# Kernel optimization log

Hardware: AMD Instinct MI355X
Metric: run time of the kernel (lower is better)

Reference implementation:

```python
import jax, jax.numpy as jnp
import numpy as np

L, HID, NH, DH, OUT = 20, 512, 8, 64, 1000
NPAT, PS = 14, 16
IN_DIM = 3 * PS * PS          # 768
SEQ = NPAT * NPAT + 1         # 197
BATCH = 64
EPS = 1e-5


def _pos_embeddings(seq_len, d):
    # sin(i/10000^(j/d)) for even j, cos(i/10000^((j-1)/d)) for odd j
    i = jnp.arange(seq_len, dtype=jnp.float32)[:, None]
    j = jnp.arange(d)
    je = (j - (j % 2)).astype(jnp.float32)
    ang = i / jnp.power(10000.0, je / d)
    return jnp.where(j % 2 == 0, jnp.sin(ang), jnp.cos(ang))


def _layernorm(x, g, b):
    m = jnp.mean(x, axis=-1, keepdims=True)
    v = jnp.mean(jnp.square(x - m), axis=-1, keepdims=True)
    return (x - m) * jax.lax.rsqrt(v + EPS) * g + b


def setup_inputs() -> dict:
    key = jax.random.key(0)
    ks = jax.random.split(key, 12)
    r = lambda k, sh: jax.random.normal(k, sh, dtype=jnp.float32) * 0.02
    return {
        "x": jax.random.normal(ks[0], (BATCH, 3, 224, 224), dtype=jnp.float32),
        "embed_W": r(ks[1], (IN_DIM, HID)),
        "embed_b": jnp.zeros((HID,), jnp.float32),
        "cls": r(ks[2], (HID,)),
        "ln1_g": jnp.ones((L, HID), jnp.float32),
        "ln1_b": jnp.zeros((L, HID), jnp.float32),
        "qW": r(ks[3], (L, NH, DH, DH)),
        "qb": jnp.zeros((L, NH, DH), jnp.float32),
        "kW": r(ks[4], (L, NH, DH, DH)),
        "kb": jnp.zeros((L, NH, DH), jnp.float32),
        "vW": r(ks[5], (L, NH, DH, DH)),
        "vb": jnp.zeros((L, NH, DH), jnp.float32),
        "ln2_g": jnp.ones((L, HID), jnp.float32),
        "ln2_b": jnp.zeros((L, HID), jnp.float32),
        "mlp1_W": r(ks[6], (L, HID, 4 * HID)),
        "mlp1_b": jnp.zeros((L, 4 * HID), jnp.float32),
        "mlp2_W": r(ks[7], (L, 4 * HID, HID)),
        "mlp2_b": jnp.zeros((L, HID), jnp.float32),
        "head_W": r(ks[8], (HID, OUT)),
        "head_b": jnp.zeros((OUT,), jnp.float32),
    }


def reference(x, embed_W, embed_b, cls, ln1_g, ln1_b, qW, qb, kW, kb, vW, vb,
              ln2_g, ln2_b, mlp1_W, mlp1_b, mlp2_W, mlp2_b, head_W, head_b):
    n = x.shape[0]
    # patchify: [n,3,224,224] -> [n,196,768], flatten order (c, ph, pw)
    p = x.reshape(n, 3, NPAT, PS, NPAT, PS)
    p = p.transpose(0, 2, 4, 1, 3, 5).reshape(n, NPAT * NPAT, IN_DIM)
    tokens = p @ embed_W + embed_b                      # [n,196,HID]
    cls_tok = jnp.broadcast_to(cls, (n, 1, HID))
    h = jnp.concatenate([cls_tok, tokens], axis=1)      # [n,197,HID]
    h = h + _pos_embeddings(SEQ, HID)

    scale = 1.0 / jnp.sqrt(jnp.float32(DH))

    def step(h, params):
        (g1, b1, qw, qb_, kw, kb_, vw, vb_, g2, b2, w1, b1m, w2, b2m) = params
        y = _layernorm(h, g1, b1)                       # [n,S,HID]
        yh = y.reshape(n, SEQ, NH, DH)
        # torch Linear: out = seq @ W.T + b; qw stored as [NH, out, in]
        q = jnp.einsum('nshd,hed->nshe', yh, qw) + qb_
        k = jnp.einsum('nshd,hed->nshe', yh, kw) + kb_
        v = jnp.einsum('nshd,hed->nshe', yh, vw) + vb_
        att = jax.nn.softmax(jnp.einsum('nqhd,nkhd->nhqk', q, k) * scale, axis=-1)
        o = jnp.einsum('nhqk,nkhd->nqhd', att, v).reshape(n, SEQ, HID)
        h = h + o
        z = _layernorm(h, g2, b2)
        z = jax.nn.gelu(z @ w1 + b1m, approximate=False) @ w2 + b2m
        return h + z, None

    params = (ln1_g, ln1_b, qW, qb, kW, kb, vW, vb,
              ln2_g, ln2_b, mlp1_W, mlp1_b, mlp2_W, mlp2_b)
    h, _ = jax.lax.scan(step, h, params)
    logits = h[:, 0] @ head_W + head_b
    return jax.nn.softmax(logits, axis=-1)
```

## Files before the change

### kernel.cpp

```cpp
#include <hip/hip_runtime.h>
#include <hip/hip_bf16.h>
#include <math.h>

#define LAY 20
#define HID 512
#define NH 8
#define DH 64
#define OUTC 1000
#define SEQ 197
#define SPAD 224
#define BATCH 64
#define TT (BATCH*SEQ)
#define M2 12800
#define NPTOK (BATCH*196)
#define IN_DIM 768

typedef __attribute__((ext_vector_type(8))) short bf16x8;
typedef __attribute__((ext_vector_type(4))) float f32x4;

__device__ __forceinline__ ushort f2bf(float f){
  __hip_bfloat16 h = __float2bfloat16(f);
  return *(ushort*)&h;
}
__device__ __forceinline__ float bf2f(ushort u){
  __hip_bfloat16 h = *(__hip_bfloat16*)&u;
  return __bfloat162float(h);
}

__device__ __forceinline__ float posemb(int i, int j){
  float je = (float)(j & ~1);
  float ang = (float)i * powf(10000.0f, -je * (1.0f/(float)HID));
  return (j & 1) ? cosf(ang) : sinf(ang);
}

__device__ __forceinline__ float gelu_exact(float x){
  return 0.5f * x * (1.0f + erff(x * 0.70710678118654752f));
}

__device__ __forceinline__ void gld_lds16(const ushort* g, ushort* l){
  __builtin_amdgcn_global_load_lds((const __attribute__((address_space(1))) void*)g,
                                   (__attribute__((address_space(3))) void*)l, 16, 0, 0);
}

__global__ __launch_bounds__(512)
void pos_kernel(float* __restrict__ pos){
  int i = blockIdx.x, j = threadIdx.x;
  pos[(size_t)i*HID + j] = posemb(i, j);
}

__global__ __launch_bounds__(256)
void convt_kernel(const float* __restrict__ src, ushort* __restrict__ dst,
                  int R, int C){
  __shared__ float tile[32][33];
  const float* s = src + (size_t)blockIdx.z * R * C;
  ushort* d      = dst + (size_t)blockIdx.z * R * C;
  int r0 = blockIdx.y * 32, c0 = blockIdx.x * 32;
  int tc = threadIdx.x & 31, tr = threadIdx.x >> 5;
  #pragma unroll
  for (int i = 0; i < 4; ++i)
    tile[tr + i*8][tc] = s[(size_t)(r0 + tr + i*8)*C + c0 + tc];
  __syncthreads();
  #pragma unroll
  for (int i = 0; i < 4; ++i)
    d[(size_t)(c0 + tr + i*8)*R + r0 + tc] = f2bf(tile[tc][tr + i*8]);
}

__global__ __launch_bounds__(256)
void cvt_kernel(const float* __restrict__ src, ushort* __restrict__ dst, int count){
  int idx = blockIdx.x * 256 + threadIdx.x;
  if (idx < count) dst[idx] = f2bf(src[idx]);
}

__global__ __launch_bounds__(256)
void patchify_kernel(const float* __restrict__ x, ushort* __restrict__ p){
  int idx = blockIdx.x * 256 + threadIdx.x;
  int r   = idx / 768, cdx = idx - r * 768;
  int n   = r / 196,  pp  = r - n * 196;
  int pr  = pp / 14,  pc  = pp - pr * 14;
  int c   = cdx >> 8, rem = cdx & 255;
  int ph  = rem >> 4, pw  = rem & 15;
  p[idx] = f2bf(x[ (((size_t)(n*3 + c)*224) + pr*16 + ph)*224 + pc*16 + pw ]);
}

__global__ __launch_bounds__(512)
void cls_kernel(const float* __restrict__ cls, const float* __restrict__ pos,
                float* __restrict__ h){
  int n = blockIdx.x, e = threadIdx.x;
  h[(size_t)n*SEQ*HID + e] = cls[e] + pos[e];
}

template<int BN, int EPI>
__global__ __launch_bounds__(256, 4)
void gemm_pipe(const ushort* __restrict__ A, const ushort* __restrict__ Bt,
               const float* __restrict__ bias, void* __restrict__ Cv,
               int K, int N, int Mreal, int NBX, const float* __restrict__ pos){
  constexpr int BM = 128;
  constexpr int MF = 4, NF = BN/32;
  constexpr int BQ = BN/64;
  constexpr int TBS = 8192 + BN*64;
  constexpr int ES = NF*16 + 12;
  __shared__ char lds[2*TBS];

  int t = threadIdx.x, lane = t & 63, wave = t >> 6;
  int wr = wave >> 1, wn = wave & 1;
  int l16 = lane & 15, g = lane >> 4;

  int NB = gridDim.x;
  int q8 = NB >> 3, r8 = NB & 7;
  int xcd = blockIdx.x & 7, i8 = blockIdx.x >> 3;
  int swz = (xcd < r8 ? xcd*(q8+1) : r8*(q8+1) + (xcd-r8)*q8) + i8;
  int rb = (swz / NBX) * BM, cb = (swz % NBX) * BN;

  const int srow = t >> 2;
  const int kel  = ((t & 3) ^ ((srow >> 1) & 3)) * 8;
  const ushort* pA[2]; const ushort* pB[BQ];
  #pragma unroll
  for (int q = 0; q < 2; ++q)
    pA[q] = A + (size_t)(rb + q*64 + srow)*K + kel;
  #pragma unroll
  for (int q = 0; q < BQ; ++q)
    pB[q] = Bt + (size_t)(cb + q*64 + srow)*K + kel;
  const int sdst = t*16;

  const int sx = (l16 >> 1) & 3;
  int aoff[MF], boff[NF];
  #pragma unroll
  for (int mf = 0; mf < MF; ++mf)
    aoff[mf] = (wr*64 + mf*16 + l16)*64 + ((g ^ sx) << 4);
  #pragma unroll
  for (int nf = 0; nf < NF; ++nf)
    boff[nf] = 8192 + (wn*(NF*16) + nf*16 + l16)*64 + ((g ^ sx) << 4);

  f32x4 acc[MF][NF];
  #pragma unroll
  for (int mf = 0; mf < MF; ++mf)
    #pragma unroll
    for (int nf = 0; nf < NF; ++nf)
      acc[mf][nf] = (f32x4){0.f,0.f,0.f,0.f};

  #pragma unroll
  for (int q = 0; q < 2; ++q)
    gld_lds16(pA[q], (ushort*)(lds + q*4096 + sdst));
  #pragma unroll
  for (int q = 0; q < BQ; ++q)
    gld_lds16(pB[q], (ushort*)(lds + 8192 + q*4096 + sdst));

  int NT = K / 32;
  for (int tt = 0; tt < NT; ++tt){
    const char* cur = lds + (tt & 1)*TBS;
    char* nxt = lds + ((tt & 1) ^ 1)*TBS;
    bool pf = (tt + 1 < NT);
    if (pf){
      const size_t kb = (size_t)(tt + 1) * 32;
      #pragma unroll
      for (int q = 0; q < 2; ++q)
        gld_lds16(pA[q] + kb, (ushort*)(nxt + q*4096 + sdst));
      #pragma unroll
      for (int q = 0; q < BQ; ++q)
        gld_lds16(pB[q] + kb, (ushort*)(nxt + 8192 + q*4096 + sdst));
      if constexpr (BQ == 2)
        asm volatile("s_waitcnt vmcnt(4)" ::: "memory");
      else
        asm volatile("s_waitcnt vmcnt(3)" ::: "memory");
    } else {
      asm volatile("s_waitcnt vmcnt(0)" ::: "memory");
    }
    __builtin_amdgcn_s_barrier();

    bf16x8 af[MF], bfr[NF];
    #pragma unroll
    for (int nf = 0; nf < NF; ++nf)
      bfr[nf] = *(const bf16x8*)(cur + boff[nf]);
    #pragma unroll
    for (int mf = 0; mf < MF; ++mf)
      af[mf] = *(const bf16x8*)(cur + aoff[mf]);

    __builtin_amdgcn_s_setprio(1);
    #pragma unroll
    for (int mf = 0; mf < MF; ++mf)
      #pragma unroll
      for (int nf = 0; nf < NF; ++nf)
        acc[mf][nf] = __builtin_amdgcn_mfma_f32_16x16x32_bf16(af[mf], bfr[nf], acc[mf][nf], 0, 0, 0);
    __builtin_amdgcn_s_setprio(0);
    __builtin_amdgcn_s_barrier();
  }

  float bvv[NF];
  #pragma unroll
  for (int nf = 0; nf < NF; ++nf)
    bvv[nf] = bias[cb + wn*(NF*16) + nf*16 + l16];
  float* eps = (float*)(lds + wave*(16*ES*4));

  #pragma unroll
  for (int mf = 0; mf < MF; ++mf){
    #pragma unroll
    for (int nf = 0; nf < NF; ++nf)
      #pragma unroll
      for (int j = 0; j < 4; ++j){
        float val = acc[mf][nf][j] + bvv[nf];
        if (EPI == 1) val = gelu_exact(val);
        eps[(g*4+j)*ES + nf*16 + l16] = val;
      }
    #pragma unroll
    for (int i = 0; i < NF; ++i){
      int id = i*64 + lane;
      int r = id / (4*NF), c4 = id % (4*NF);
      float4 vv = *(float4*)&eps[r*ES + c4*4];
      int grow = rb + wr*64 + mf*16 + r;
      int gcol = cb + wn*(NF*16) + c4*4;
      if (EPI == 1){
        ushort4 u;
        u.x = f2bf(vv.x); u.y = f2bf(vv.y); u.z = f2bf(vv.z); u.w = f2bf(vv.w);
        *(ushort4*)&((ushort*)Cv)[(size_t)grow*N + gcol] = u;
      } else if (EPI == 2){
        if (grow < Mreal){
          float* cp = &((float*)Cv)[(size_t)grow*N + gcol];
          float4 o = *(float4*)cp;
          o.x += vv.x; o.y += vv.y; o.z += vv.z; o.w += vv.w;
          *(float4*)cp = o;
        }
      } else {
        if (grow < Mreal){
          int bn = grow / 196, sp = grow - bn*196;
          float4 pv = *(const float4*)&pos[(size_t)(1+sp)*HID + gcol];
          vv.x += pv.x; vv.y += pv.y; vv.z += pv.z; vv.w += pv.w;
          *(float4*)&((float*)Cv)[((size_t)bn*SEQ + 1 + sp)*HID + gcol] = vv;
        }
      }
    }
  }
}

__global__ __launch_bounds__(128)
void ln_kernel(const float* __restrict__ x, const float* __restrict__ g,
               const float* __restrict__ b, ushort* __restrict__ y){
  int tok = blockIdx.x, t = threadIdx.x;
  int wave = t >> 6;
  __shared__ float red[2];
  float4 v = *(const float4*)&x[(size_t)tok*HID + t*4];
  float s = (v.x + v.y) + (v.z + v.w);
  #pragma unroll
  for (int off = 32; off; off >>= 1) s += __shfl_xor(s, off);
  if ((t & 63) == 0) red[wave] = s;
  __syncthreads();
  float mean = (red[0] + red[1]) * (1.0f/512.0f);
  __syncthreads();
  float dx = v.x - mean, dy = v.y - mean, dz = v.z - mean, dw = v.w - mean;
  s = (dx*dx + dy*dy) + (dz*dz + dw*dw);
  #pragma unroll
  for (int off = 32; off; off >>= 1) s += __shfl_xor(s, off);
  if ((t & 63) == 0) red[wave] = s;
  __syncthreads();
  float var = (red[0] + red[1]) * (1.0f/512.0f);
  float rs  = rsqrtf(var + 1e-5f);
  float4 gv = *(const float4*)&g[t*4];
  float4 bv = *(const float4*)&b[t*4];
  ushort4 o;
  o.x = f2bf(dx*rs*gv.x + bv.x);
  o.y = f2bf(dy*rs*gv.y + bv.y);
  o.z = f2bf(dz*rs*gv.z + bv.z);
  o.w = f2bf(dw*rs*gv.w + bv.w);
  *(ushort4*)&y[(size_t)tok*HID + t*4] = o;
}

__global__ __launch_bounds__(256)
void qkv_mfma(const ushort* __restrict__ y,
              const ushort* __restrict__ wqb, const ushort* __restrict__ wkb,
              const ushort* __restrict__ wvb,
              const float* __restrict__ bq, const float* __restrict__ bk,
              const float* __restrict__ bv,
              ushort* __restrict__ q, ushort* __restrict__ k,
              ushort* __restrict__ v){
  __shared__ short As[128*64];
  __shared__ short Bs[3][64*64];
  int t = threadIdx.x;
  int lane = t & 63, wave = t >> 6;
  int l16 = lane & 15, g = lane >> 4;
  int hh = blockIdx.y;
  int rb = blockIdx.x * 128;

  const ushort* Wp[3] = { wqb + (size_t)hh*64*64, wkb + (size_t)hh*64*64, wvb + (size_t)hh*64*64 };
  const float* biasp[3] = { bq + hh*64, bk + hh*64, bv + hh*64 };
  ushort* outp[3] = { q, k, v };

  int srow = t >> 3, skoff = (t & 7) * 8;
  const ushort* Ab = y + (size_t)(rb + srow)*HID + hh*64 + skoff;
  #pragma unroll
  for (int i = 0; i < 4; ++i)
    gld_lds16(Ab + (size_t)(i*32)*HID, (ushort*)&As[t*8 + i*2048]);
  #pragma unroll
  for (int p = 0; p < 3; ++p){
    const ushort* Bb = Wp[p] + (size_t)srow*64 + skoff;
    #pragma unroll
    for (int i = 0; i < 2; ++i)
      gld_lds16(Bb + (size_t)(i*32)*64, (ushort*)&Bs[p][t*8 + i*2048]);
  }
  __syncthreads();

  bf16x8 af[2][2];
  #pragma unroll
  for (int kc = 0; kc < 2; ++kc)
    #pragma unroll
    for (int m = 0; m < 2; ++m)
      af[kc][m] = *(bf16x8*)&As[(wave*32 + m*16 + l16)*64 + kc*32 + g*8];
  __syncthreads();

  ushort* eps = (ushort*)As + wave*(16*72);
  #pragma unroll
  for (int p = 0; p < 3; ++p){
    f32x4 acc[2][4];
    #pragma unroll
    for (int m = 0; m < 2; ++m)
      #pragma unroll
      for (int n = 0; n < 4; ++n)
        acc[m][n] = (f32x4){0.f,0.f,0.f,0.f};
    #pragma unroll
    for (int kc = 0; kc < 2; ++kc){
      bf16x8 bfr[4];
      #pragma unroll
      for (int n = 0; n < 4; ++n)
        bfr[n] = *(bf16x8*)&Bs[p][(n*16 + l16)*64 + kc*32 + g*8];
      #pragma unroll
      for (int m = 0; m < 2; ++m)
        #pragma unroll
        for (int n = 0; n < 4; ++n)
          acc[m][n] = __builtin_amdgcn_mfma_f32_16x16x32_bf16(af[kc][m], bfr[n], acc[m][n], 0, 0, 0);
    }
    float bvv[4];
    #pragma unroll
    for (int nd = 0; nd < 4; ++nd) bvv[nd] = biasp[p][nd*16 + l16];
    ushort* out = outp[p];
    #pragma unroll
    for (int mch = 0; mch < 2; ++mch){
      #pragma unroll
      for (int nd = 0; nd < 4; ++nd)
        #pragma unroll
        for (int j = 0; j < 4; ++j)
          eps[(g*4+j)*72 + nd*16 + l16] = f2bf(acc[mch][nd][j] + bvv[nd]);
      #pragma unroll
      for (int i = 0; i < 2; ++i){
        int id = i*64 + lane;
        int r = id >> 3, c8 = id & 7;
        uint4 vv = *(uint4*)&eps[r*72 + c8*8];
        int tok = rb + wave*32 + mch*16 + r;
        if (tok < TT)
          *(uint4*)&out[(size_t)tok*HID + hh*64 + c8*8] = vv;
      }
    }
  }
}

__global__ __launch_bounds__(512, 4)
void attn_kernel(const ushort* __restrict__ q, const ushort* __restrict__ k,
                 const ushort* __restrict__ v, float* __restrict__ h){
  __shared__ ushort Ks[SPAD*64];
  __shared__ ushort Vs[64*256];
  __shared__ ushort Ps[8][32*40];
  int nh = blockIdx.x;
  int n = nh >> 3, hd = nh & 7;
  int t = threadIdx.x;
  int lane = t & 63, wave = t >> 6;
  int l16 = lane & 15, g = lane >> 4;

  const ushort* kbase = k + ((size_t)n*SEQ)*HID + hd*64;
  for (int c = t; c < 224*8; c += 512){
    int s = c >> 3, c8 = (c & 7) * 8;
    int sr = s < SEQ ? s : SEQ-1;
    uint4 val = *(const uint4*)&kbase[(size_t)sr*HID + c8];
    int byte = s*128 + c8*2;
    byte ^= (s & 7) << 4;
    *(uint4*)((char*)Ks + byte) = val;
  }
  const ushort* vbase = v + ((size_t)n*SEQ)*HID + hd*64;
  for (int c = t; c < 224*8; c += 512){
    int s = c >> 3, d8 = (c & 7) * 8;
    uint4 val = {0u,0u,0u,0u};
    if (s < SEQ) val = *(const uint4*)&vbase[(size_t)s*HID + d8];
    ushort* vsp = (ushort*)Vs;
    #pragma unroll
    for (int e = 0; e < 8; ++e){
      int d = d8 + e;
      int swzi = ((d & 7) ^ ((d >> 3) & 7)) << 4;
      int byte = d*512 + ((s*2) ^ swzi);
      vsp[byte >> 1] = ((ushort*)&val)[e];
    }
  }

  int qrow0 = wave * 32;
  bool wactive = qrow0 < SEQ;
  bf16x8 aq[2][2];
  if (wactive){
    #pragma unroll
    for (int m = 0; m < 2; ++m){
      int row = qrow0 + m*16 + l16;
      int sr = row < SEQ ? row : SEQ-1;
      const ushort* qp = q + ((size_t)n*SEQ + sr)*HID + hd*64;
      #pragma unroll
      for (int kc = 0; kc < 2; ++kc)
        aq[m][kc] = *(const bf16x8*)&qp[kc*32 + g*8];
    }
  }
  __syncthreads();

  if (wactive){
    ushort* myP = &Ps[wave][0];
    f32x4 accO[2][4];
    float mrun[2][4], lrun[2][4];
    #pragma unroll
    for (int m = 0; m < 2; ++m){
      #pragma unroll
      for (int nd = 0; nd < 4; ++nd) accO[m][nd] = (f32x4){0.f,0.f,0.f,0.f};
      #pragma unroll
      for (int j = 0; j < 4; ++j){ mrun[m][j] = -1e30f; lrun[m][j] = 0.f; }
    }

    for (int kt = 0; kt < 7; ++kt){
      f32x4 accS[2][2];
      #pragma unroll
      for (int m = 0; m < 2; ++m)
        #pragma unroll
        for (int nn = 0; nn < 2; ++nn) accS[m][nn] = (f32x4){0.f,0.f,0.f,0.f};
      #pragma unroll
      for (int kc = 0; kc < 2; ++kc){
        bf16x8 bk[2];
        #pragma unroll
        for (int nn = 0; nn < 2; ++nn){
          int srow = kt*32 + nn*16 + l16;
          int byte = srow*128 + kc*64 + g*16;
          byte ^= (srow & 7) << 4;
          bk[nn] = *(const bf16x8*)((const char*)Ks + byte);
        }
        #pragma unroll
        for (int m = 0; m < 2; ++m)
          #pragma unroll
          for (int nn = 0; nn < 2; ++nn)
            accS[m][nn] = __builtin_amdgcn_mfma_f32_16x16x32_bf16(aq[m][kc], bk[nn], accS[m][nn], 0, 0, 0);
      }
      bool kv0 = (kt*32 + l16) < SEQ;
      bool kv1 = (kt*32 + 16 + l16) < SEQ;
      #pragma unroll
      for (int m = 0; m < 2; ++m){
        #pragma unroll
        for (int j = 0; j < 4; ++j){
          float s0 = kv0 ? accS[m][0][j]*0.125f : -1e30f;
          float s1 = kv1 ? accS[m][1][j]*0.125f : -1e30f;
          float mx = fmaxf(s0, s1);
          mx = fmaxf(mx, __shfl_xor(mx, 1));
          mx = fmaxf(mx, __shfl_xor(mx, 2));
          mx = fmaxf(mx, __shfl_xor(mx, 4));
          mx = fmaxf(mx, __shfl_xor(mx, 8));
          float mold = mrun[m][j];
          float mnew = fmaxf(mold, mx);
          float corr = __expf(mold - mnew);
          mrun[m][j] = mnew;
          float p0 = __expf(s0 - mnew);
          float p1 = __expf(s1 - mnew);
          float rs = p0 + p1;
          rs += __shfl_xor(rs, 1);
          rs += __shfl_xor(rs, 2);
          rs += __shfl_xor(rs, 4);
          rs += __shfl_xor(rs, 8);
          lrun[m][j] = lrun[m][j]*corr + rs;
          #pragma unroll
          for (int nd = 0; nd < 4; ++nd) accO[m][nd][j] *= corr;
          int prow = m*16 + g*4 + j;
          myP[prow*40 + l16]      = f2bf(p0);
          myP[prow*40 + 16 + l16] = f2bf(p1);
        }
      }
      bf16x8 ap[2], bv[4];
      #pragma unroll
      for (int m = 0; m < 2; ++m)
        ap[m] = *(const bf16x8*)&myP[(m*16 + l16)*40 + g*8];
      #pragma unroll
      for (int nd = 0; nd < 4; ++nd){
        int d = nd*16 + l16;
        int byte = d*512 + kt*64 + g*16;
        byte ^= ((d & 7) ^ ((d >> 3) & 7)) << 4;
        bv[nd] = *(const bf16x8*)((const char*)Vs + byte);
      }
      #pragma unroll
      for (int m = 0; m < 2; ++m)
        #pragma unroll
        for (int nd = 0; nd < 4; ++nd)
          accO[m][nd] = __builtin_amdgcn_mfma_f32_16x16x32_bf16(ap[m], bv[nd], accO[m][nd], 0, 0, 0);
    }

    #pragma unroll
    for (int m = 0; m < 2; ++m){
      #pragma unroll
      for (int j = 0; j < 4; ++j){
        int row = qrow0 + m*16 + g*4 + j;
        if (row < SEQ){
          float inv = 1.0f / lrun[m][j];
          float* hp = h + ((size_t)n*SEQ + row)*HID + hd*64;
          #pragma unroll
          for (int nd = 0; nd < 4; ++nd)
            hp[nd*16 + l16] += accO[m][nd][j] * inv;
        }
      }
    }
  }
}

__global__ __launch_bounds__(256)
void head_logits(const float* __restrict__ h, const float* __restrict__ W,
                 const float* __restrict__ b, float* __restrict__ logits){
  int c0 = blockIdx.x * 8;
  __shared__ float Ws[512*8];
  int t = threadIdx.x;
  for (int i = t; i < 512*8; i += 256){
    int kx = i >> 3, c = i & 7;
    Ws[i] = W[(size_t)kx*OUTC + c0 + c];
  }
  __syncthreads();
  int n = t >> 2, g = t & 3;
  const float* hp = h + (size_t)n*SEQ*HID + g*128;
  float acc[8] = {};
  for (int kx = 0; kx < 128; ++kx){
    float hv = hp[kx];
    const float* wsr = &Ws[(g*128 + kx)*8];
    #pragma unroll
    for (int c = 0; c < 8; ++c) acc[c] += hv * wsr[c];
  }
  #pragma unroll
  for (int c = 0; c < 8; ++c){
    acc[c] += __shfl_xor(acc[c], 1);
    acc[c] += __shfl_xor(acc[c], 2);
  }
  if (g == 0){
    #pragma unroll
    for (int c = 0; c < 8; ++c)
      logits[(size_t)n*OUTC + c0 + c] = acc[c] + b[c0 + c];
  }
}

__global__ __launch_bounds__(256)
void head_softmax(const float* __restrict__ logits, float* __restrict__ out){
  int n = blockIdx.x, t = threadIdx.x;
  __shared__ float red[4];
  float v[4];
  #pragma unroll
  for (int j = 0; j < 4; ++j){
    int e = t + j*256;
    v[j] = (e < OUTC) ? logits[(size_t)n*OUTC + e] : -1e30f;
  }
  float mx = fmaxf(fmaxf(v[0], v[1]), fmaxf(v[2], v[3]));
  #pragma unroll
  for (int off = 32; off; off >>= 1) mx = fmaxf(mx, __shfl_xor(mx, off));
  if ((t & 63) == 0) red[t >> 6] = mx;
  __syncthreads();
  mx = fmaxf(fmaxf(red[0], red[1]), fmaxf(red[2], red[3]));
  __syncthreads();
  float sum = 0.f;
  #pragma unroll
  for (int j = 0; j < 4; ++j){ v[j] = __expf(v[j] - mx); sum += v[j]; }
  #pragma unroll
  for (int off = 32; off; off >>= 1) sum += __shfl_xor(sum, off);
  if ((t & 63) == 0) red[t >> 6] = sum;
  __syncthreads();
  sum = red[0] + red[1] + red[2] + red[3];
  float inv = 1.0f / sum;
  #pragma unroll
  for (int j = 0; j < 4; ++j){
    int e = t + j*256;
    if (e < OUTC) out[(size_t)n*OUTC + e] = v[j] * inv;
  }
}

extern "C" void kernel_launch(void* const* d_in, const int* in_sizes, int n_in,
                              void* d_out, int out_size, void* d_ws, size_t ws_size,
                              hipStream_t stream){
  const float* x       = (const float*)d_in[0];
  const float* embed_W = (const float*)d_in[1];
  const float* embed_b = (const float*)d_in[2];
  const float* cls     = (const float*)d_in[3];
  const float* ln1_g   = (const float*)d_in[4];
  const float* ln1_b   = (const float*)d_in[5];
  const float* qW      = (const float*)d_in[6];
  const float* qb      = (const float*)d_in[7];
  const float* kW      = (const float*)d_in[8];
  const float* kb      = (const float*)d_in[9];
  const float* vW      = (const float*)d_in[10];
  const float* vb      = (const float*)d_in[11];
  const float* ln2_g   = (const float*)d_in[12];
  const float* ln2_b   = (const float*)d_in[13];
  const float* mlp1_W  = (const float*)d_in[14];
  const float* mlp1_b  = (const float*)d_in[15];
  const float* mlp2_W  = (const float*)d_in[16];
  const float* mlp2_b  = (const float*)d_in[17];
  const float* head_W  = (const float*)d_in[18];
  const float* head_b  = (const float*)d_in[19];
  float* out = (float*)d_out;

  char* wsb = (char*)d_ws;
  float*  h   = (float*)wsb;
  ushort* y   = (ushort*)(wsb + (size_t)M2*HID*4);
  float*  logits = (float*)y;
  char*   un  = wsb + (size_t)M2*HID*4 + (size_t)M2*HID*2;
  ushort* qb_  = (ushort*)un;
  ushort* kb_  = qb_ + (size_t)TT*HID;
  ushort* vb_  = kb_ + (size_t)TT*HID;
  ushort* z1  = (ushort*)un;
  ushort* p   = (ushort*)un;
  char*   wts = un + (size_t)3*TT*HID*4;
  ushort* w1t = (ushort*)wts;
  ushort* w2t = w1t + (size_t)LAY*2048*512;
  ushort* wet = w2t + (size_t)LAY*2048*512;
  ushort* wqb = wet + (size_t)IN_DIM*HID;
  ushort* wkb = wqb + (size_t)LAY*NH*DH*DH;
  ushort* wvb = wkb + (size_t)LAY*NH*DH*DH;
  float*  pos = (float*)(wvb + (size_t)LAY*NH*DH*DH);

  pos_kernel<<<SEQ, 512, 0, stream>>>(pos);
  convt_kernel<<<dim3(2048/32, 512/32, LAY), 256, 0, stream>>>(mlp1_W, w1t, 512, 2048);
  convt_kernel<<<dim3(512/32, 2048/32, LAY), 256, 0, stream>>>(mlp2_W, w2t, 2048, 512);
  convt_kernel<<<dim3(512/32, 768/32, 1),    256, 0, stream>>>(embed_W, wet, 768, 512);
  {
    int cnt = LAY*NH*DH*DH;
    int grd = (cnt + 255)/256;
    cvt_kernel<<<grd, 256, 0, stream>>>(qW, wqb, cnt);
    cvt_kernel<<<grd, 256, 0, stream>>>(kW, wkb, cnt);
    cvt_kernel<<<grd, 256, 0, stream>>>(vW, wvb, cnt);
  }

  patchify_kernel<<<(NPTOK*IN_DIM)/256, 256, 0, stream>>>(x, p);
  cls_kernel<<<BATCH, 512, 0, stream>>>(cls, pos, h);
  gemm_pipe<128, 3><<<(512/128)*(M2/128), 256, 0, stream>>>(
      p, wet, embed_b, h, IN_DIM, HID, NPTOK, 512/128, pos);

  for (int l = 0; l < LAY; ++l){
    ln_kernel<<<TT, 128, 0, stream>>>(h, ln1_g + l*HID, ln1_b + l*HID, y);
    qkv_mfma<<<dim3(M2/128, 8), 256, 0, stream>>>(
        y,
        wqb + (size_t)l*NH*DH*DH, wkb + (size_t)l*NH*DH*DH, wvb + (size_t)l*NH*DH*DH,
        qb + (size_t)l*HID, kb + (size_t)l*HID, vb + (size_t)l*HID,
        qb_, kb_, vb_);
    attn_kernel<<<BATCH*NH, 512, 0, stream>>>(qb_, kb_, vb_, h);
    ln_kernel<<<TT, 128, 0, stream>>>(h, ln2_g + l*HID, ln2_b + l*HID, y);
    gemm_pipe<128, 1><<<(2048/128)*(M2/128), 256, 0, stream>>>(
        y, w1t + (size_t)l*2048*512, mlp1_b + (size_t)l*4*HID, z1,
        HID, 4*HID, TT, 2048/128, pos);
    gemm_pipe<128, 2><<<(512/128)*(M2/128), 256, 0, stream>>>(
        z1, w2t + (size_t)l*2048*512, mlp2_b + (size_t)l*HID, h,
        4*HID, HID, TT, 512/128, pos);
  }

  head_logits<<<125, 256, 0, stream>>>(h, head_W, head_b, logits);
  head_softmax<<<BATCH, 256, 0, stream>>>(logits, out);
}
```

Before: 3.170 ms.

## Load GEMM B-operand fragments directly from global into registers, bypassing LDS

```diff
diff --git a/kernel.cpp b/kernel.cpp
--- a/kernel.cpp
+++ b/kernel.cpp
@@ -89,17 +89,16 @@
   h[(size_t)n*SEQ*HID + e] = cls[e] + pos[e];
 }
 
-template<int BN, int EPI>
+template<int EPI>
 __global__ __launch_bounds__(256, 4)
 void gemm_pipe(const ushort* __restrict__ A, const ushort* __restrict__ Bt,
                const float* __restrict__ bias, void* __restrict__ Cv,
                int K, int N, int Mreal, int NBX, const float* __restrict__ pos){
-  constexpr int BM = 128;
-  constexpr int MF = 4, NF = BN/32;
-  constexpr int BQ = BN/64;
-  constexpr int TBS = 8192 + BN*64;
-  constexpr int ES = NF*16 + 12;
-  __shared__ char lds[2*TBS];
+  constexpr int BM = 128, BN = 128;
+  constexpr int MF = 4, NF = 4;
+  constexpr int TBS = 8192;
+  constexpr int ES = 76;
+  __shared__ char lds[20480];
 
   int t = threadIdx.x, lane = t & 63, wave = t >> 6;
   int wr = wave >> 1, wn = wave & 1;
@@ -113,23 +112,22 @@
 
   const int srow = t >> 2;
   const int kel  = ((t & 3) ^ ((srow >> 1) & 3)) * 8;
-  const ushort* pA[2]; const ushort* pB[BQ];
+  const ushort* pA[2];
   #pragma unroll
   for (int q = 0; q < 2; ++q)
     pA[q] = A + (size_t)(rb + q*64 + srow)*K + kel;
-  #pragma unroll
-  for (int q = 0; q < BQ; ++q)
-    pB[q] = Bt + (size_t)(cb + q*64 + srow)*K + kel;
   const int sdst = t*16;
 
   const int sx = (l16 >> 1) & 3;
-  int aoff[MF], boff[NF];
+  int aoff[MF];
   #pragma unroll
   for (int mf = 0; mf < MF; ++mf)
     aoff[mf] = (wr*64 + mf*16 + l16)*64 + ((g ^ sx) << 4);
+
+  const ushort* bgp[NF];
   #pragma unroll
   for (int nf = 0; nf < NF; ++nf)
-    boff[nf] = 8192 + (wn*(NF*16) + nf*16 + l16)*64 + ((g ^ sx) << 4);
+    bgp[nf] = Bt + (size_t)(cb + wn*64 + nf*16 + l16)*K + g*8;
 
   f32x4 acc[MF][NF];
   #pragma unroll
@@ -141,36 +139,31 @@
   #pragma unroll
   for (int q = 0; q < 2; ++q)
     gld_lds16(pA[q], (ushort*)(lds + q*4096 + sdst));
-  #pragma unroll
-  for (int q = 0; q < BQ; ++q)
-    gld_lds16(pB[q], (ushort*)(lds + 8192 + q*4096 + sdst));
 
   int NT = K / 32;
   for (int tt = 0; tt < NT; ++tt){
     const char* cur = lds + (tt & 1)*TBS;
     char* nxt = lds + ((tt & 1) ^ 1)*TBS;
+
+    bf16x8 bfr[NF];
+    #pragma unroll
+    for (int nf = 0; nf < NF; ++nf)
+      bfr[nf] = *(const bf16x8*)(bgp[nf] + tt*32);
+    asm volatile("" ::: "memory");
+
     bool pf = (tt + 1 < NT);
     if (pf){
       const size_t kb = (size_t)(tt + 1) * 32;
       #pragma unroll
       for (int q = 0; q < 2; ++q)
         gld_lds16(pA[q] + kb, (ushort*)(nxt + q*4096 + sdst));
-      #pragma unroll
-      for (int q = 0; q < BQ; ++q)
-        gld_lds16(pB[q] + kb, (ushort*)(nxt + 8192 + q*4096 + sdst));
-      if constexpr (BQ == 2)
-        asm volatile("s_waitcnt vmcnt(4)" ::: "memory");
-      else
-        asm volatile("s_waitcnt vmcnt(3)" ::: "memory");
+      asm volatile("s_waitcnt vmcnt(2)" ::: "memory");
     } else {
       asm volatile("s_waitcnt vmcnt(0)" ::: "memory");
     }
     __builtin_amdgcn_s_barrier();
 
-    bf16x8 af[MF], bfr[NF];
-    #pragma unroll
-    for (int nf = 0; nf < NF; ++nf)
-      bfr[nf] = *(const bf16x8*)(cur + boff[nf]);
+    bf16x8 af[MF];
     #pragma unroll
     for (int mf = 0; mf < MF; ++mf)
       af[mf] = *(const bf16x8*)(cur + aoff[mf]);
@@ -188,7 +181,7 @@
   float bvv[NF];
   #pragma unroll
   for (int nf = 0; nf < NF; ++nf)
-    bvv[nf] = bias[cb + wn*(NF*16) + nf*16 + l16];
+    bvv[nf] = bias[cb + wn*64 + nf*16 + l16];
   float* eps = (float*)(lds + wave*(16*ES*4));
 
   #pragma unroll
@@ -202,12 +195,12 @@
         eps[(g*4+j)*ES + nf*16 + l16] = val;
       }
     #pragma unroll
-    for (int i = 0; i < NF; ++i){
+    for (int i = 0; i < 4; ++i){
       int id = i*64 + lane;
-      int r = id / (4*NF), c4 = id % (4*NF);
+      int r = id >> 4, c4 = id & 15;
       float4 vv = *(float4*)&eps[r*ES + c4*4];
       int grow = rb + wr*64 + mf*16 + r;
-      int gcol = cb + wn*(NF*16) + c4*4;
+      int gcol = cb + wn*64 + c4*4;
       if (EPI == 1){
         ushort4 u;
         u.x = f2bf(vv.x); u.y = f2bf(vv.y); u.z = f2bf(vv.z); u.w = f2bf(vv.w);
@@ -626,7 +619,7 @@
 
   patchify_kernel<<<(NPTOK*IN_DIM)/256, 256, 0, stream>>>(x, p);
   cls_kernel<<<BATCH, 512, 0, stream>>>(cls, pos, h);
-  gemm_pipe<128, 3><<<(512/128)*(M2/128), 256, 0, stream>>>(
+  gemm_pipe<3><<<(512/128)*(M2/128), 256, 0, stream>>>(
       p, wet, embed_b, h, IN_DIM, HID, NPTOK, 512/128, pos);
 
   for (int l = 0; l < LAY; ++l){
@@ -638,10 +631,10 @@
         qb_, kb_, vb_);
     attn_kernel<<<BATCH*NH, 512, 0, stream>>>(qb_, kb_, vb_, h);
     ln_kernel<<<TT, 128, 0, stream>>>(h, ln2_g + l*HID, ln2_b + l*HID, y);
-    gemm_pipe<128, 1><<<(2048/128)*(M2/128), 256, 0, stream>>>(
+    gemm_pipe<1><<<(2048/128)*(M2/128), 256, 0, stream>>>(
         y, w1t + (size_t)l*2048*512, mlp1_b + (size_t)l*4*HID, z1,
         HID, 4*HID, TT, 2048/128, pos);
-    gemm_pipe<128, 2><<<(512/128)*(M2/128), 256, 0, stream>>>(
+    gemm_pipe<2><<<(512/128)*(M2/128), 256, 0, stream>>>(
         z1, w2t + (size_t)l*2048*512, mlp2_b + (size_t)l*HID, h,
         4*HID, HID, TT, 512/128, pos);
   }
```

New measurement: 4.306 ms. +35.8%, slower.
